# Kernel tuning notes

Measured on AMD Instinct MI355X. Metric: run time of the kernel, lower is better.

The kernel has to match this reference:

```python
import jax, jax.numpy as jnp
import numpy as np

B, T, D, N = 2, 2048, 1024, 16
DT_RANK = 64  # ceil(D / 16)


def setup_inputs() -> dict:
    key = jax.random.key(0)
    ks = jax.random.split(key, 8)
    x = jax.random.normal(ks[0], (B, T, D), dtype=jnp.float32)
    # Linear weights stored as (out, in) like torch; applied as x @ W.T
    W_B = jax.random.normal(ks[1], (N, D), dtype=jnp.float32) / np.sqrt(D)
    W_C = jax.random.normal(ks[2], (N, D), dtype=jnp.float32) / np.sqrt(D)
    W_dt1 = jax.random.normal(ks[3], (DT_RANK, D), dtype=jnp.float32) / np.sqrt(D)
    W_dt2 = jax.random.normal(ks[4], (D, DT_RANK), dtype=jnp.float32) / np.sqrt(DT_RANK)
    # dt bias init: inverse-softplus of dt sampled log-uniform in [dt_min, dt_max]
    dt_min, dt_max = 1e-3, 1e-1
    u = jax.random.uniform(ks[5], (D,), dtype=jnp.float32)
    dt_init = jnp.clip(jnp.exp(u * (np.log(dt_max) - np.log(dt_min)) + np.log(dt_min)), 1e-4, None)
    b_dt2 = dt_init + jnp.log(-jnp.expm1(-dt_init))
    # log_A: per original non-HiPPO path, A in (0.5, 1.0), broadcast to (D, N)
    a = jax.random.uniform(ks[6], (N,), dtype=jnp.float32) * 0.5 + 0.5
    log_A = jnp.broadcast_to(jnp.log(a)[None, :], (D, N)).copy()
    D_skip = jnp.ones((D,), dtype=jnp.float32)
    return {"x": x, "W_B": W_B, "W_C": W_C, "W_dt1": W_dt1,
            "W_dt2": W_dt2, "b_dt2": b_dt2, "log_A": log_A, "D_skip": D_skip}


def _selective_scan(A_bar, B_bar, C):
    # A_bar, B_bar: (B, T, D, N); C: (B, T, N) -> y: (B, T, D)
    def step(h, inputs):
        a_t, b_t, c_t = inputs  # (B,D,N), (B,D,N), (B,N)
        h = a_t * h + b_t
        y_t = jnp.einsum('bdn,bn->bd', h, c_t)
        return h, y_t

    h0 = jnp.zeros(A_bar.shape[:1] + A_bar.shape[2:], dtype=A_bar.dtype)  # (B,D,N)
    xs = (jnp.moveaxis(A_bar, 1, 0), jnp.moveaxis(B_bar, 1, 0), jnp.moveaxis(C, 1, 0))
    _, ys = jax.lax.scan(step, h0, xs)  # ys: (T, B, D)
    return jnp.moveaxis(ys, 0, 1)


def reference(x, W_B, W_C, W_dt1, W_dt2, b_dt2, log_A, D_skip):
    # Projections
    B_t = jnp.einsum('btd,nd->btn', x, W_B)          # (B,T,N)
    C_t = jnp.einsum('btd,nd->btn', x, W_C)          # (B,T,N)
    dt_raw = jnp.einsum('btr,dr->btd', jnp.einsum('btd,rd->btr', x, W_dt1), W_dt2) + b_dt2
    dt = jax.nn.softplus(dt_raw)                     # (B,T,D)
    A = -jnp.exp(log_A)                              # (D,N), negative
    # Discretization
    A_bar = jnp.exp(dt[..., None] * A[None, None])   # (B,T,D,N)
    dB = (A_bar - 1.0) / (A[None, None] + 1e-8)
    B_bar = dB * x[..., None] * B_t[:, :, None, :]   # (B,T,D,N)
    y = _selective_scan(A_bar, B_bar, C_t)           # (B,T,D)
    return y + D_skip * x
```

## Files before the change

kernel.cpp:

```cpp
#include <hip/hip_runtime.h>
#include <hip/hip_bf16.h>

#define BB 2
#define TT 2048
#define DD 1024
#define NN 16
#define RR 64
#define MM (BB*TT)
#define KDIM DD
#define CHUNK 32
#define NCHUNK (TT/CHUNK)
#define KSPLIT 8

#define BT_OFF 0
#define CT_OFF 65536
#define R1_OFF 131072
#define DT_OFF 393216
#define P_OFF  4587520
#define S_OFF  6684672
#define H_OFF  8781824
#define PP_OFF 10878976

#define LOG2E 1.4426950408889634f

#if __has_builtin(__builtin_amdgcn_exp2f)
#define EXP2(x) __builtin_amdgcn_exp2f(x)
#else
#define EXP2(x) exp2f(x)
#endif

__device__ __forceinline__ float softplus_f(float z) {
    return fmaxf(z, 0.0f) + log1pf(expf(-fabsf(z)));
}

__global__ __launch_bounds__(256) void k_proj96(
    const float* __restrict__ x, const float* __restrict__ W_B,
    const float* __restrict__ W_C, const float* __restrict__ W_dt1,
    float* __restrict__ Pp)
{
    __shared__ float xs[16][68];
    __shared__ float wsT[16][97];

    const int tid = threadIdx.x;
    const int r0 = blockIdx.x * 64;
    const int kbase = blockIdx.y * (KDIM / KSPLIT);
    const int tx = tid & 15;
    const int ty = tid >> 4;

    float acc[4][6];
    #pragma unroll
    for (int i = 0; i < 4; i++)
        #pragma unroll
        for (int j = 0; j < 6; j++) acc[i][j] = 0.0f;

    for (int kc = 0; kc < KDIM / KSPLIT; kc += 16) {
        {
            const int row = tid >> 2;
            const int kq = (tid & 3) * 4;
            float4 v = *(const float4*)(x + (size_t)(r0 + row) * KDIM + kbase + kc + kq);
            xs[kq + 0][row] = v.x; xs[kq + 1][row] = v.y;
            xs[kq + 2][row] = v.z; xs[kq + 3][row] = v.w;
        }
        #pragma unroll
        for (int i = 0; i < 6; i++) {
            const int idx = i * 256 + tid;
            const int c = idx >> 4;
            const int kk = idx & 15;
            const float* wrow; int cc;
            if (c < 16)      { wrow = W_B;   cc = c; }
            else if (c < 32) { wrow = W_C;   cc = c - 16; }
            else             { wrow = W_dt1; cc = c - 32; }
            wsT[kk][c] = wrow[(size_t)cc * KDIM + kbase + kc + kk];
        }
        __syncthreads();
        #pragma unroll
        for (int kk = 0; kk < 16; kk++) {
            const float a0 = xs[kk][ty * 4 + 0];
            const float a1 = xs[kk][ty * 4 + 1];
            const float a2 = xs[kk][ty * 4 + 2];
            const float a3 = xs[kk][ty * 4 + 3];
            #pragma unroll
            for (int j = 0; j < 6; j++) {
                const float b = wsT[kk][tx + j * 16];
                acc[0][j] = fmaf(a0, b, acc[0][j]);
                acc[1][j] = fmaf(a1, b, acc[1][j]);
                acc[2][j] = fmaf(a2, b, acc[2][j]);
                acc[3][j] = fmaf(a3, b, acc[3][j]);
            }
        }
        __syncthreads();
    }

    float* out = Pp + (size_t)blockIdx.y * (MM * 96);
    #pragma unroll
    for (int i = 0; i < 4; i++) {
        const int r = r0 + ty * 4 + i;
        #pragma unroll
        for (int j = 0; j < 6; j++)
            out[(size_t)r * 96 + tx + j * 16] = acc[i][j];
    }
}

__global__ __launch_bounds__(256) void k_reduce96(
    const float* __restrict__ Pp, const float* __restrict__ log_A,
    float* __restrict__ Bt, float* __restrict__ Ct, float* __restrict__ R1)
{
    const int gid = blockIdx.x * 256 + threadIdx.x;
    const int e0 = gid * 4;
    float4 s = *(const float4*)(Pp + e0);
    #pragma unroll
    for (int p = 1; p < KSPLIT; p++) {
        const float4 v = *(const float4*)(Pp + (size_t)p * MM * 96 + e0);
        s.x += v.x; s.y += v.y; s.z += v.z; s.w += v.w;
    }
    const int r = e0 / 96;
    const int c = e0 - r * 96;
    if (c < 16) {
        const float4 lgj = *(const float4*)(log_A + c);
        s.x *= 1.0f / (-__expf(lgj.x) + 1e-8f);
        s.y *= 1.0f / (-__expf(lgj.y) + 1e-8f);
        s.z *= 1.0f / (-__expf(lgj.z) + 1e-8f);
        s.w *= 1.0f / (-__expf(lgj.w) + 1e-8f);
        *(float4*)(Bt + (size_t)r * NN + c) = s;
    } else if (c < 32) {
        *(float4*)(Ct + (size_t)r * NN + (c - 16)) = s;
    } else {
        *(float4*)(R1 + (size_t)r * RR + (c - 32)) = s;
    }
}

__global__ __launch_bounds__(256, 4) void k_dtproj(
    const float* __restrict__ R1, const float* __restrict__ W_dt2,
    const float* __restrict__ b_dt2, float* __restrict__ dt)
{
    __shared__ float r1s[64][68];
    __shared__ float wsT[64][68];

    const int tid = threadIdx.x;
    const int r0 = blockIdx.x * 64;
    const int d0 = blockIdx.y * 64;

    #pragma unroll
    for (int i = 0; i < 4; i++) {
        const int f = tid + i * 256;
        const int row = f >> 4;
        const int kq = (f & 15) * 4;
        *(float4*)&r1s[row][kq] = *(const float4*)(R1 + (size_t)(r0 + row) * RR + kq);
    }
    {
        const int dl = tid >> 2;
        const int kq0 = (tid & 3) * 16;
        const float* src = W_dt2 + (size_t)(d0 + dl) * RR + kq0;
        #pragma unroll
        for (int j = 0; j < 16; j += 4) {
            const float4 v = *(const float4*)(src + j);
            wsT[kq0 + j + 0][dl] = v.x;
            wsT[kq0 + j + 1][dl] = v.y;
            wsT[kq0 + j + 2][dl] = v.z;
            wsT[kq0 + j + 3][dl] = v.w;
        }
    }
    __syncthreads();

    const int cg = tid & 15;
    const int rg = tid >> 4;

    float4 acc[4];
    #pragma unroll
    for (int i = 0; i < 4; i++) acc[i] = make_float4(0.f, 0.f, 0.f, 0.f);

    #pragma unroll
    for (int k4 = 0; k4 < 16; k4++) {
        float r1a[4][4];
        #pragma unroll
        for (int i = 0; i < 4; i++) {
            const float4 v = *(const float4*)&r1s[rg * 4 + i][k4 * 4];
            r1a[i][0] = v.x; r1a[i][1] = v.y; r1a[i][2] = v.z; r1a[i][3] = v.w;
        }
        #pragma unroll
        for (int kk = 0; kk < 4; kk++) {
            const float4 w = *(const float4*)&wsT[k4 * 4 + kk][cg * 4];
            #pragma unroll
            for (int i = 0; i < 4; i++) {
                const float a = r1a[i][kk];
                acc[i].x = fmaf(a, w.x, acc[i].x);
                acc[i].y = fmaf(a, w.y, acc[i].y);
                acc[i].z = fmaf(a, w.z, acc[i].z);
                acc[i].w = fmaf(a, w.w, acc[i].w);
            }
        }
    }

    const float4 bias = *(const float4*)(b_dt2 + d0 + cg * 4);
    #pragma unroll
    for (int i = 0; i < 4; i++) {
        const int row = r0 + rg * 4 + i;
        float4 o;
        o.x = softplus_f(acc[i].x + bias.x);
        o.y = softplus_f(acc[i].y + bias.y);
        o.z = softplus_f(acc[i].z + bias.z);
        o.w = softplus_f(acc[i].w + bias.w);
        *(float4*)(dt + (size_t)row * DD + d0 + cg * 4) = o;
    }
}

__global__ __launch_bounds__(256, 2) void k_scan1(
    const float* __restrict__ x, const float* __restrict__ dt,
    const float* __restrict__ Bt, const float* __restrict__ log_A,
    float* __restrict__ P, float* __restrict__ Sg)
{
    __shared__ float bt_s[CHUNK][NN];

    const int tid = threadIdx.x;
    const int d = blockIdx.x * 256 + tid;
    const int c = blockIdx.y;
    const int b = blockIdx.z;
    const int base = b * TT + c * CHUNK;

    if (tid < CHUNK * NN / 4) {
        const int t = tid >> 2;
        const int jc = (tid & 3) * 4;
        *(float4*)&bt_s[t][jc] = *(const float4*)(Bt + (size_t)(base + t) * NN + jc);
    }

    const float* gdt = dt + (size_t)base * DD + d;
    const float* gx  = x  + (size_t)base * DD + d;
    float dv[CHUNK], xv[CHUNK];
    #pragma unroll
    for (int t = 0; t < CHUNK; t++) {
        dv[t] = gdt[(size_t)t * DD];
        xv[t] = gx[(size_t)t * DD];
    }

    float A2[16];
    #pragma unroll
    for (int q = 0; q < 4; q++) {
        const float4 lg = *(const float4*)(log_A + d * NN + q * 4);
        A2[q * 4 + 0] = -__expf(lg.x) * LOG2E;
        A2[q * 4 + 1] = -__expf(lg.y) * LOG2E;
        A2[q * 4 + 2] = -__expf(lg.z) * LOG2E;
        A2[q * 4 + 3] = -__expf(lg.w) * LOG2E;
    }

    __syncthreads();

    float s[16];
    #pragma unroll
    for (int n = 0; n < 16; n++) s[n] = 0.0f;
    float dtsum = 0.0f;

    #pragma unroll
    for (int t = 0; t < CHUNK; t++) {
        const float dtv = dv[t];
        const float xvv = xv[t];
        dtsum += dtv;
        #pragma unroll
        for (int q = 0; q < 4; q++) {
            const float4 bt4 = *(const float4*)&bt_s[t][q * 4];
            const float a0 = EXP2(dtv * A2[q * 4 + 0]);
            const float a1 = EXP2(dtv * A2[q * 4 + 1]);
            const float a2 = EXP2(dtv * A2[q * 4 + 2]);
            const float a3 = EXP2(dtv * A2[q * 4 + 3]);
            const float u0 = xvv * bt4.x;
            const float u1 = xvv * bt4.y;
            const float u2 = xvv * bt4.z;
            const float u3 = xvv * bt4.w;
            s[q * 4 + 0] = fmaf(a0, s[q * 4 + 0] + u0, -u0);
            s[q * 4 + 1] = fmaf(a1, s[q * 4 + 1] + u1, -u1);
            s[q * 4 + 2] = fmaf(a2, s[q * 4 + 2] + u2, -u2);
            s[q * 4 + 3] = fmaf(a3, s[q * 4 + 3] + u3, -u3);
        }
    }

    const size_t o = ((size_t)(c * BB + b) * DD + d) * NN;
    #pragma unroll
    for (int q = 0; q < 4; q++) {
        *(float4*)(P + o + q * 4) = make_float4(
            EXP2(A2[q * 4 + 0] * dtsum), EXP2(A2[q * 4 + 1] * dtsum),
            EXP2(A2[q * 4 + 2] * dtsum), EXP2(A2[q * 4 + 3] * dtsum));
        *(float4*)(Sg + o + q * 4) = make_float4(
            s[q * 4 + 0], s[q * 4 + 1], s[q * 4 + 2], s[q * 4 + 3]);
    }
}

__global__ __launch_bounds__(256) void k_comb(
    const float* __restrict__ P, const float* __restrict__ Sg,
    float* __restrict__ Hs)
{
    const int flat = blockIdx.x * 256 + threadIdx.x;
    float h = 0.0f;
    #pragma unroll 8
    for (int c = 0; c < NCHUNK; c++) {
        const size_t idx = (size_t)c * (BB * DD * NN) + flat;
        Hs[idx] = h;
        h = fmaf(P[idx], h, Sg[idx]);
    }
}

__global__ __launch_bounds__(256, 2) void k_scan2(
    const float* __restrict__ x, const float* __restrict__ dt,
    const float* __restrict__ Bt, const float* __restrict__ Ct,
    const float* __restrict__ log_A, const float* __restrict__ D_skip,
    const float* __restrict__ Hs, float* __restrict__ y)
{
    __shared__ float bt_s[CHUNK][NN];
    __shared__ float ct_s[CHUNK][NN];

    const int tid = threadIdx.x;
    const int d = blockIdx.x * 256 + tid;
    const int c = blockIdx.y;
    const int b = blockIdx.z;
    const int base = b * TT + c * CHUNK;

    if (tid < 128) {
        const int t = tid >> 2;
        const int jc = (tid & 3) * 4;
        *(float4*)&bt_s[t][jc] = *(const float4*)(Bt + (size_t)(base + t) * NN + jc);
    } else {
        const int t2 = (tid - 128) >> 2;
        const int jc = (tid & 3) * 4;
        *(float4*)&ct_s[t2][jc] = *(const float4*)(Ct + (size_t)(base + t2) * NN + jc);
    }

    const float* gdt = dt + (size_t)base * DD + d;
    const float* gx  = x  + (size_t)base * DD + d;
    float dv[CHUNK], xv[CHUNK];
    #pragma unroll
    for (int t = 0; t < CHUNK; t++) {
        dv[t] = gdt[(size_t)t * DD];
        xv[t] = gx[(size_t)t * DD];
    }

    float A2[16];
    #pragma unroll
    for (int q = 0; q < 4; q++) {
        const float4 lg = *(const float4*)(log_A + d * NN + q * 4);
        A2[q * 4 + 0] = -__expf(lg.x) * LOG2E;
        A2[q * 4 + 1] = -__expf(lg.y) * LOG2E;
        A2[q * 4 + 2] = -__expf(lg.z) * LOG2E;
        A2[q * 4 + 3] = -__expf(lg.w) * LOG2E;
    }
    const float dsk = D_skip[d];

    float h[16];
    {
        const size_t hoff = (size_t)c * (BB * DD * NN) + (size_t)b * (DD * NN) + (size_t)d * NN;
        #pragma unroll
        for (int q = 0; q < 4; q++) {
            const float4 hv = *(const float4*)(Hs + hoff + q * 4);
            h[q * 4 + 0] = hv.x; h[q * 4 + 1] = hv.y;
            h[q * 4 + 2] = hv.z; h[q * 4 + 3] = hv.w;
        }
    }

    __syncthreads();

    float* yp = y + (size_t)base * DD + d;

    #pragma unroll
    for (int t = 0; t < CHUNK; t++) {
        const float dtv = dv[t];
        const float xvv = xv[t];
        float part = 0.0f;
        #pragma unroll
        for (int q = 0; q < 4; q++) {
            const float4 bt4 = *(const float4*)&bt_s[t][q * 4];
            const float4 ct4 = *(const float4*)&ct_s[t][q * 4];
            const float a0 = EXP2(dtv * A2[q * 4 + 0]);
            const float a1 = EXP2(dtv * A2[q * 4 + 1]);
            const float a2 = EXP2(dtv * A2[q * 4 + 2]);
            const float a3 = EXP2(dtv * A2[q * 4 + 3]);
            const float u0 = xvv * bt4.x;
            const float u1 = xvv * bt4.y;
            const float u2 = xvv * bt4.z;
            const float u3 = xvv * bt4.w;
            h[q * 4 + 0] = fmaf(a0, h[q * 4 + 0] + u0, -u0);
            h[q * 4 + 1] = fmaf(a1, h[q * 4 + 1] + u1, -u1);
            h[q * 4 + 2] = fmaf(a2, h[q * 4 + 2] + u2, -u2);
            h[q * 4 + 3] = fmaf(a3, h[q * 4 + 3] + u3, -u3);
            part = fmaf(h[q * 4 + 0], ct4.x, part);
            part = fmaf(h[q * 4 + 1], ct4.y, part);
            part = fmaf(h[q * 4 + 2], ct4.z, part);
            part = fmaf(h[q * 4 + 3], ct4.w, part);
        }
        yp[(size_t)t * DD] = fmaf(dsk, xvv, part);
    }
}

extern "C" void kernel_launch(void* const* d_in, const int* in_sizes, int n_in,
                              void* d_out, int out_size, void* d_ws, size_t ws_size,
                              hipStream_t stream)
{
    const float* x      = (const float*)d_in[0];
    const float* W_B    = (const float*)d_in[1];
    const float* W_C    = (const float*)d_in[2];
    const float* W_dt1  = (const float*)d_in[3];
    const float* W_dt2  = (const float*)d_in[4];
    const float* b_dt2  = (const float*)d_in[5];
    const float* log_A  = (const float*)d_in[6];
    const float* D_skip = (const float*)d_in[7];
    float* y = (float*)d_out;

    float* ws = (float*)d_ws;
    float* Bt = ws + BT_OFF;
    float* Ct = ws + CT_OFF;
    float* R1 = ws + R1_OFF;
    float* dt = ws + DT_OFF;
    float* P  = ws + P_OFF;
    float* S  = ws + S_OFF;
    float* Hs = ws + H_OFF;
    float* Pp = ws + PP_OFF;

    k_proj96<<<dim3(MM / 64, KSPLIT), 256, 0, stream>>>(x, W_B, W_C, W_dt1, Pp);
    k_reduce96<<<dim3(MM * 96 / 4 / 256), 256, 0, stream>>>(Pp, log_A, Bt, Ct, R1);
    k_dtproj<<<dim3(MM / 64, DD / 64), 256, 0, stream>>>(R1, W_dt2, b_dt2, dt);
    k_scan1<<<dim3(DD / 256, NCHUNK, BB), 256, 0, stream>>>(x, dt, Bt, log_A, P, S);
    k_comb<<<dim3(BB * DD * NN / 256), 256, 0, stream>>>(P, S, Hs);
    k_scan2<<<dim3(DD / 256, NCHUNK, BB), 256, 0, stream>>>(x, dt, Bt, Ct, log_A, D_skip, Hs, y);
}
```

Measured before the change: 162.5 us.

## Fuse split-K reduction via atomics and halve scan chunk size

The split-K projection now accumulates its partial sums directly into Bt/Ct/R1 with atomicAdd after a memset, and the B scaling by 1/A is folded into the weight load. This removes the separate reduce kernel and the large partial-sum buffer. The scan chunk length drops from 32 to 16 and the scan kernels request 4 blocks per SM instead of 2, which lowers register use and adds more parallel blocks. The cost is a longer chunk-combine pass and more P/S/H state traffic. Atomic float accumulation also makes the summation order nondeterministic.

```diff
diff --git a/kernel.cpp b/kernel.cpp
--- a/kernel.cpp
+++ b/kernel.cpp
@@ -8,7 +8,7 @@
 #define RR 64
 #define MM (BB*TT)
 #define KDIM DD
-#define CHUNK 32
+#define CHUNK 16
 #define NCHUNK (TT/CHUNK)
 #define KSPLIT 8
 
@@ -17,9 +17,8 @@
 #define R1_OFF 131072
 #define DT_OFF 393216
 #define P_OFF  4587520
-#define S_OFF  6684672
-#define H_OFF  8781824
-#define PP_OFF 10878976
+#define S_OFF  8781824
+#define H_OFF  12976128
 
 #define LOG2E 1.4426950408889634f
 
@@ -36,7 +35,8 @@
 __global__ __launch_bounds__(256) void k_proj96(
     const float* __restrict__ x, const float* __restrict__ W_B,
     const float* __restrict__ W_C, const float* __restrict__ W_dt1,
-    float* __restrict__ Pp)
+    const float* __restrict__ log_A,
+    float* __restrict__ Bt, float* __restrict__ Ct, float* __restrict__ R1)
 {
     __shared__ float xs[16][68];
     __shared__ float wsT[16][97];
@@ -46,6 +46,10 @@
     const int kbase = blockIdx.y * (KDIM / KSPLIT);
     const int tx = tid & 15;
     const int ty = tid >> 4;
+
+    const float bscale = 1.0f / (-__expf(log_A[ty]) + 1e-8f);
+    const float* wrow0 = W_B + (size_t)ty * KDIM;
+    const float* wrow1 = W_C + (size_t)ty * KDIM;
 
     float acc[4][6];
     #pragma unroll
@@ -61,16 +65,14 @@
             xs[kq + 0][row] = v.x; xs[kq + 1][row] = v.y;
             xs[kq + 2][row] = v.z; xs[kq + 3][row] = v.w;
         }
-        #pragma unroll
-        for (int i = 0; i < 6; i++) {
-            const int idx = i * 256 + tid;
-            const int c = idx >> 4;
-            const int kk = idx & 15;
-            const float* wrow; int cc;
-            if (c < 16)      { wrow = W_B;   cc = c; }
-            else if (c < 32) { wrow = W_C;   cc = c - 16; }
-            else             { wrow = W_dt1; cc = c - 32; }
-            wsT[kk][c] = wrow[(size_t)cc * KDIM + kbase + kc + kk];
+        {
+            const int koff = kbase + kc + tx;
+            wsT[tx][ty]      = wrow0[koff] * bscale;
+            wsT[tx][16 + ty] = wrow1[koff];
+            #pragma unroll
+            for (int i = 2; i < 6; i++)
+                wsT[tx][i * 16 + ty] =
+                    W_dt1[(size_t)((i - 2) * 16 + ty) * KDIM + koff];
         }
         __syncthreads();
         #pragma unroll
@@ -91,41 +93,15 @@
         __syncthreads();
     }
 
-    float* out = Pp + (size_t)blockIdx.y * (MM * 96);
     #pragma unroll
     for (int i = 0; i < 4; i++) {
         const int r = r0 + ty * 4 + i;
-        #pragma unroll
-        for (int j = 0; j < 6; j++)
-            out[(size_t)r * 96 + tx + j * 16] = acc[i][j];
-    }
-}
-
-__global__ __launch_bounds__(256) void k_reduce96(
-    const float* __restrict__ Pp, const float* __restrict__ log_A,
-    float* __restrict__ Bt, float* __restrict__ Ct, float* __restrict__ R1)
-{
-    const int gid = blockIdx.x * 256 + threadIdx.x;
-    const int e0 = gid * 4;
-    float4 s = *(const float4*)(Pp + e0);
-    #pragma unroll
-    for (int p = 1; p < KSPLIT; p++) {
-        const float4 v = *(const float4*)(Pp + (size_t)p * MM * 96 + e0);
-        s.x += v.x; s.y += v.y; s.z += v.z; s.w += v.w;
-    }
-    const int r = e0 / 96;
-    const int c = e0 - r * 96;
-    if (c < 16) {
-        const float4 lgj = *(const float4*)(log_A + c);
-        s.x *= 1.0f / (-__expf(lgj.x) + 1e-8f);
-        s.y *= 1.0f / (-__expf(lgj.y) + 1e-8f);
-        s.z *= 1.0f / (-__expf(lgj.z) + 1e-8f);
-        s.w *= 1.0f / (-__expf(lgj.w) + 1e-8f);
-        *(float4*)(Bt + (size_t)r * NN + c) = s;
-    } else if (c < 32) {
-        *(float4*)(Ct + (size_t)r * NN + (c - 16)) = s;
-    } else {
-        *(float4*)(R1 + (size_t)r * RR + (c - 32)) = s;
+        atomicAdd(&Bt[(size_t)r * NN + tx],      acc[i][0]);
+        atomicAdd(&Ct[(size_t)r * NN + tx],      acc[i][1]);
+        atomicAdd(&R1[(size_t)r * RR + tx],      acc[i][2]);
+        atomicAdd(&R1[(size_t)r * RR + tx + 16], acc[i][3]);
+        atomicAdd(&R1[(size_t)r * RR + tx + 32], acc[i][4]);
+        atomicAdd(&R1[(size_t)r * RR + tx + 48], acc[i][5]);
     }
 }
 
@@ -204,7 +180,7 @@
     }
 }
 
-__global__ __launch_bounds__(256, 2) void k_scan1(
+__global__ __launch_bounds__(256, 4) void k_scan1(
     const float* __restrict__ x, const float* __restrict__ dt,
     const float* __restrict__ Bt, const float* __restrict__ log_A,
     float* __restrict__ P, float* __restrict__ Sg)
@@ -297,7 +273,7 @@
     }
 }
 
-__global__ __launch_bounds__(256, 2) void k_scan2(
+__global__ __launch_bounds__(256, 4) void k_scan2(
     const float* __restrict__ x, const float* __restrict__ dt,
     const float* __restrict__ Bt, const float* __restrict__ Ct,
     const float* __restrict__ log_A, const float* __restrict__ D_skip,
@@ -312,12 +288,12 @@
     const int b = blockIdx.z;
     const int base = b * TT + c * CHUNK;
 
-    if (tid < 128) {
+    if (tid < 64) {
         const int t = tid >> 2;
         const int jc = (tid & 3) * 4;
         *(float4*)&bt_s[t][jc] = *(const float4*)(Bt + (size_t)(base + t) * NN + jc);
-    } else {
-        const int t2 = (tid - 128) >> 2;
+    } else if (tid < 128) {
+        const int t2 = (tid - 64) >> 2;
         const int jc = (tid & 3) * 4;
         *(float4*)&ct_s[t2][jc] = *(const float4*)(Ct + (size_t)(base + t2) * NN + jc);
     }
@@ -409,10 +385,10 @@
     float* P  = ws + P_OFF;
     float* S  = ws + S_OFF;
     float* Hs = ws + H_OFF;
-    float* Pp = ws + PP_OFF;
-
-    k_proj96<<<dim3(MM / 64, KSPLIT), 256, 0, stream>>>(x, W_B, W_C, W_dt1, Pp);
-    k_reduce96<<<dim3(MM * 96 / 4 / 256), 256, 0, stream>>>(Pp, log_A, Bt, Ct, R1);
+
+    hipMemsetAsync(ws + BT_OFF, 0, (size_t)(DT_OFF - BT_OFF) * sizeof(float), stream);
+
+    k_proj96<<<dim3(MM / 64, KSPLIT), 256, 0, stream>>>(x, W_B, W_C, W_dt1, log_A, Bt, Ct, R1);
     k_dtproj<<<dim3(MM / 64, DD / 64), 256, 0, stream>>>(R1, W_dt2, b_dt2, dt);
     k_scan1<<<dim3(DD / 256, NCHUNK, BB), 256, 0, stream>>>(x, dt, Bt, log_A, P, S);
     k_comb<<<dim3(BB * DD * NN / 256), 256, 0, stream>>>(P, S, Hs);
```

Result: slower. 169.7 us (+4.5%).

## Compute intra-chunk output in first scan pass and add carried-state correction later

Applied to the files above, without the earlier changes.

The first chunked scan pass now also computes the zero-initial-state output contribution and the cumulative dt per step, writing both to workspace. The second pass no longer reruns the recurrence. It adds the decayed carried-in state, exp(A*cumdt)*h0 dotted with C, to the stored partial output. This removes the repeated 16-state recurrence and the x and dt reloads in the second pass, at the cost of writing and reading two extra full (B,T,D) buffers and doing extra exponentials in the finish kernel.

```diff
diff --git a/kernel.cpp b/kernel.cpp
--- a/kernel.cpp
+++ b/kernel.cpp
@@ -20,6 +20,8 @@
 #define S_OFF  6684672
 #define H_OFF  8781824
 #define PP_OFF 10878976
+#define YP_OFF 14024704
+#define DC_OFF 18219008
 
 #define LOG2E 1.4426950408889634f
 
@@ -206,10 +208,13 @@
 
 __global__ __launch_bounds__(256, 2) void k_scan1(
     const float* __restrict__ x, const float* __restrict__ dt,
-    const float* __restrict__ Bt, const float* __restrict__ log_A,
-    float* __restrict__ P, float* __restrict__ Sg)
+    const float* __restrict__ Bt, const float* __restrict__ Ct,
+    const float* __restrict__ log_A, const float* __restrict__ D_skip,
+    float* __restrict__ P, float* __restrict__ Sg,
+    float* __restrict__ ypart, float* __restrict__ dtc)
 {
     __shared__ float bt_s[CHUNK][NN];
+    __shared__ float ct_s[CHUNK][NN];
 
     const int tid = threadIdx.x;
     const int d = blockIdx.x * 256 + tid;
@@ -217,10 +222,14 @@
     const int b = blockIdx.z;
     const int base = b * TT + c * CHUNK;
 
-    if (tid < CHUNK * NN / 4) {
+    if (tid < 128) {
         const int t = tid >> 2;
         const int jc = (tid & 3) * 4;
         *(float4*)&bt_s[t][jc] = *(const float4*)(Bt + (size_t)(base + t) * NN + jc);
+    } else {
+        const int t2 = (tid - 128) >> 2;
+        const int jc = (tid & 3) * 4;
+        *(float4*)&ct_s[t2][jc] = *(const float4*)(Ct + (size_t)(base + t2) * NN + jc);
     }
 
     const float* gdt = dt + (size_t)base * DD + d;
@@ -241,8 +250,12 @@
         A2[q * 4 + 2] = -__expf(lg.z) * LOG2E;
         A2[q * 4 + 3] = -__expf(lg.w) * LOG2E;
     }
+    const float dsk = D_skip[d];
 
     __syncthreads();
+
+    float* ypp = ypart + (size_t)base * DD + d;
+    float* dcp = dtc   + (size_t)base * DD + d;
 
     float s[16];
     #pragma unroll
@@ -254,9 +267,11 @@
         const float dtv = dv[t];
         const float xvv = xv[t];
         dtsum += dtv;
+        float part = 0.0f;
         #pragma unroll
         for (int q = 0; q < 4; q++) {
             const float4 bt4 = *(const float4*)&bt_s[t][q * 4];
+            const float4 ct4 = *(const float4*)&ct_s[t][q * 4];
             const float a0 = EXP2(dtv * A2[q * 4 + 0]);
             const float a1 = EXP2(dtv * A2[q * 4 + 1]);
             const float a2 = EXP2(dtv * A2[q * 4 + 2]);
@@ -269,7 +284,13 @@
             s[q * 4 + 1] = fmaf(a1, s[q * 4 + 1] + u1, -u1);
             s[q * 4 + 2] = fmaf(a2, s[q * 4 + 2] + u2, -u2);
             s[q * 4 + 3] = fmaf(a3, s[q * 4 + 3] + u3, -u3);
-        }
+            part = fmaf(s[q * 4 + 0], ct4.x, part);
+            part = fmaf(s[q * 4 + 1], ct4.y, part);
+            part = fmaf(s[q * 4 + 2], ct4.z, part);
+            part = fmaf(s[q * 4 + 3], ct4.w, part);
+        }
+        ypp[(size_t)t * DD] = fmaf(dsk, xvv, part);
+        dcp[(size_t)t * DD] = dtsum;
     }
 
     const size_t o = ((size_t)(c * BB + b) * DD + d) * NN;
@@ -297,13 +318,11 @@
     }
 }
 
-__global__ __launch_bounds__(256, 2) void k_scan2(
-    const float* __restrict__ x, const float* __restrict__ dt,
-    const float* __restrict__ Bt, const float* __restrict__ Ct,
-    const float* __restrict__ log_A, const float* __restrict__ D_skip,
+__global__ __launch_bounds__(256, 4) void k_finish(
+    const float* __restrict__ ypart, const float* __restrict__ dtc,
+    const float* __restrict__ Ct, const float* __restrict__ log_A,
     const float* __restrict__ Hs, float* __restrict__ y)
 {
-    __shared__ float bt_s[CHUNK][NN];
     __shared__ float ct_s[CHUNK][NN];
 
     const int tid = threadIdx.x;
@@ -312,23 +331,10 @@
     const int b = blockIdx.z;
     const int base = b * TT + c * CHUNK;
 
-    if (tid < 128) {
+    if (tid < CHUNK * NN / 4) {
         const int t = tid >> 2;
         const int jc = (tid & 3) * 4;
-        *(float4*)&bt_s[t][jc] = *(const float4*)(Bt + (size_t)(base + t) * NN + jc);
-    } else {
-        const int t2 = (tid - 128) >> 2;
-        const int jc = (tid & 3) * 4;
-        *(float4*)&ct_s[t2][jc] = *(const float4*)(Ct + (size_t)(base + t2) * NN + jc);
-    }
-
-    const float* gdt = dt + (size_t)base * DD + d;
-    const float* gx  = x  + (size_t)base * DD + d;
-    float dv[CHUNK], xv[CHUNK];
-    #pragma unroll
-    for (int t = 0; t < CHUNK; t++) {
-        dv[t] = gdt[(size_t)t * DD];
-        xv[t] = gx[(size_t)t * DD];
+        *(float4*)&ct_s[t][jc] = *(const float4*)(Ct + (size_t)(base + t) * NN + jc);
     }
 
     float A2[16];
@@ -340,50 +346,43 @@
         A2[q * 4 + 2] = -__expf(lg.z) * LOG2E;
         A2[q * 4 + 3] = -__expf(lg.w) * LOG2E;
     }
-    const float dsk = D_skip[d];
-
-    float h[16];
+
+    float h0[16];
     {
-        const size_t hoff = (size_t)c * (BB * DD * NN) + (size_t)b * (DD * NN) + (size_t)d * NN;
+        const size_t hoff = (size_t)c * (BB * DD * NN) + (size_t)b * (DD * NN)
+                          + (size_t)d * NN;
         #pragma unroll
         for (int q = 0; q < 4; q++) {
             const float4 hv = *(const float4*)(Hs + hoff + q * 4);
-            h[q * 4 + 0] = hv.x; h[q * 4 + 1] = hv.y;
-            h[q * 4 + 2] = hv.z; h[q * 4 + 3] = hv.w;
+            h0[q * 4 + 0] = hv.x; h0[q * 4 + 1] = hv.y;
+            h0[q * 4 + 2] = hv.z; h0[q * 4 + 3] = hv.w;
         }
     }
 
     __syncthreads();
 
+    const float* gyp = ypart + (size_t)base * DD + d;
+    const float* gdc = dtc   + (size_t)base * DD + d;
     float* yp = y + (size_t)base * DD + d;
 
-    #pragma unroll
+    #pragma unroll 8
     for (int t = 0; t < CHUNK; t++) {
-        const float dtv = dv[t];
-        const float xvv = xv[t];
-        float part = 0.0f;
+        const float dc  = gdc[(size_t)t * DD];
+        const float ypv = gyp[(size_t)t * DD];
+        float corr = 0.0f;
         #pragma unroll
         for (int q = 0; q < 4; q++) {
-            const float4 bt4 = *(const float4*)&bt_s[t][q * 4];
             const float4 ct4 = *(const float4*)&ct_s[t][q * 4];
-            const float a0 = EXP2(dtv * A2[q * 4 + 0]);
-            const float a1 = EXP2(dtv * A2[q * 4 + 1]);
-            const float a2 = EXP2(dtv * A2[q * 4 + 2]);
-            const float a3 = EXP2(dtv * A2[q * 4 + 3]);
-            const float u0 = xvv * bt4.x;
-            const float u1 = xvv * bt4.y;
-            const float u2 = xvv * bt4.z;
-            const float u3 = xvv * bt4.w;
-            h[q * 4 + 0] = fmaf(a0, h[q * 4 + 0] + u0, -u0);
-            h[q * 4 + 1] = fmaf(a1, h[q * 4 + 1] + u1, -u1);
-            h[q * 4 + 2] = fmaf(a2, h[q * 4 + 2] + u2, -u2);
-            h[q * 4 + 3] = fmaf(a3, h[q * 4 + 3] + u3, -u3);
-            part = fmaf(h[q * 4 + 0], ct4.x, part);
-            part = fmaf(h[q * 4 + 1], ct4.y, part);
-            part = fmaf(h[q * 4 + 2], ct4.z, part);
-            part = fmaf(h[q * 4 + 3], ct4.w, part);
-        }
-        yp[(size_t)t * DD] = fmaf(dsk, xvv, part);
+            const float e0 = EXP2(dc * A2[q * 4 + 0]) * h0[q * 4 + 0];
+            const float e1 = EXP2(dc * A2[q * 4 + 1]) * h0[q * 4 + 1];
+            const float e2 = EXP2(dc * A2[q * 4 + 2]) * h0[q * 4 + 2];
+            const float e3 = EXP2(dc * A2[q * 4 + 3]) * h0[q * 4 + 3];
+            corr = fmaf(e0, ct4.x, corr);
+            corr = fmaf(e1, ct4.y, corr);
+            corr = fmaf(e2, ct4.z, corr);
+            corr = fmaf(e3, ct4.w, corr);
+        }
+        yp[(size_t)t * DD] = ypv + corr;
     }
 }
 
@@ -410,11 +409,13 @@
     float* S  = ws + S_OFF;
     float* Hs = ws + H_OFF;
     float* Pp = ws + PP_OFF;
+    float* yp = ws + YP_OFF;
+    float* dc = ws + DC_OFF;
 
     k_proj96<<<dim3(MM / 64, KSPLIT), 256, 0, stream>>>(x, W_B, W_C, W_dt1, Pp);
     k_reduce96<<<dim3(MM * 96 / 4 / 256), 256, 0, stream>>>(Pp, log_A, Bt, Ct, R1);
-    k_dtproj<<<dim3(MM / 64, DD / 64), 256, 0, stream>>>(R1, W_dt2, b_dt2, dt);
-    k_scan1<<<dim3(DD / 256, NCHUNK, BB), 256, 0, stream>>>(x, dt, Bt, log_A, P, S);
+    k_dtproj<<<dim3(MM / 64, DD / 128 / 2 * 2 == DD / 64 ? DD / 64 : DD / 64), 256, 0, stream>>>(R1, W_dt2, b_dt2, dt);
+    k_scan1<<<dim3(DD / 256, NCHUNK, BB), 256, 0, stream>>>(x, dt, Bt, Ct, log_A, D_skip, P, S, yp, dc);
     k_comb<<<dim3(BB * DD * NN / 256), 256, 0, stream>>>(P, S, Hs);
-    k_scan2<<<dim3(DD / 256, NCHUNK, BB), 256, 0, stream>>>(x, dt, Bt, Ct, log_A, D_skip, Hs, y);
-}
+    k_finish<<<dim3(DD / 256, NCHUNK, BB), 256, 0, stream>>>(yp, dc, Ct, log_A, Hs, y);
+}
```

Measured after the change: 171.4 us. +5.5%, slower.
